# Kernel tuning notes

Measured on AMD Instinct MI355X. Metric: run time of the kernel, lower is better.

The kernel has to match this reference:

```python
import jax, jax.numpy as jnp
import numpy as np

NEG = 1e12  # matches torch code's -1e12 masking constant


def _rope_sincos(seq_len, dim, dtype):
    # SinusoidalPositionEmbedding with merge_mode='zero':
    # emb[n, i] pairs -> reshape to [n, dim] as [sin0, cos0, sin1, cos1, ...]
    pos = jnp.arange(seq_len, dtype=jnp.float32)
    inv = jnp.power(10000.0, -2.0 * jnp.arange(dim // 2, dtype=jnp.float32) / dim)
    ang = pos[:, None] * inv[None, :]            # [n, d/2]
    sin, cos = jnp.sin(ang), jnp.cos(ang)
    # cos_pos = pos[..., 1::2].repeat_interleave(2) == repeat(cos, 2)
    cos_pos = jnp.repeat(cos, 2, axis=-1).astype(dtype)  # [n, d]
    sin_pos = jnp.repeat(sin, 2, axis=-1).astype(dtype)  # [n, d]
    return sin_pos, cos_pos


def _rotate_half(x):
    # stack([-x[..., 1::2], x[..., ::2]], -1).reshape(x.shape)
    x2 = jnp.stack([-x[..., 1::2], x[..., ::2]], axis=-1)
    return x2.reshape(x.shape)


def setup_inputs() -> dict:
    key = jax.random.key(0)
    k1, k2, k3 = jax.random.split(key, 3)
    B, N, H = 8, 1024, 768
    heads, head_size = 12, 64
    inputs = jax.random.normal(k1, (B, N, H), dtype=jnp.float32)
    mask = jnp.ones((B, N), dtype=jnp.float32)
    W = jax.random.normal(k2, (H, heads * head_size * 2), dtype=jnp.float32) * (H ** -0.5)
    b = jnp.zeros((heads * head_size * 2,), dtype=jnp.float32)
    return {"inputs": inputs, "mask": mask, "W": W, "b": b}


def reference(inputs, mask, W, b):
    heads, head_size = 12, 64
    B, N, _ = inputs.shape
    x = inputs @ W + b                              # [B, N, heads*head_size*2]
    x = x.reshape(B, N, heads, 2 * head_size)       # split+stack over heads
    qw, kw = x[..., :head_size], x[..., head_size:]  # [B, N, heads, d]

    sin_pos, cos_pos = _rope_sincos(N, head_size, inputs.dtype)
    sin_pos = sin_pos[None, :, None, :]             # [1, N, 1, d]
    cos_pos = cos_pos[None, :, None, :]
    qw = qw * cos_pos + _rotate_half(qw) * sin_pos
    kw = kw * cos_pos + _rotate_half(kw) * sin_pos

    logits = jnp.einsum('bmhd,bnhd->bhmn', qw, kw)  # [B, heads, N, N]

    m1 = mask[:, None, :, None]                     # mask rows (axis ndim-2)
    m2 = mask[:, None, None, :]                     # mask cols (axis ndim-1)
    logits = logits * m1 + (-NEG) * (1.0 - m1)
    logits = logits * m2 + (-NEG) * (1.0 - m2)
    tril = jnp.tril(jnp.ones((N, N), dtype=logits.dtype), k=-1)
    logits = logits - tril * NEG                    # forbid end < start
    return logits / (head_size ** 0.5)
```

## Files before the change

kernel.cpp:

```cpp
#include <hip/hip_runtime.h>
#include <stdint.h>

#define NEGC 1000000000000.0f

using f32x4  = __attribute__((ext_vector_type(4))) float;
using short8 = __attribute__((ext_vector_type(8))) short;

typedef __attribute__((address_space(3))) uint32_t* lds_ptr_t;
typedef const __attribute__((address_space(1))) uint32_t* gptr_t;

__device__ __forceinline__ void gload_lds16(const void* g, const void* l) {
  __builtin_amdgcn_global_load_lds((gptr_t)g, (lds_ptr_t)l, 16, 0, 0);
}

__device__ __forceinline__ unsigned short f2bf(float f) {
  union { float f; uint32_t u; } v; v.f = f;
  uint32_t u = v.u;
  return (unsigned short)((u + 0x7fffu + ((u >> 16) & 1u)) >> 16);
}

__global__ __launch_bounds__(256) void k_prep(
    const float* __restrict__ in, unsigned short* __restrict__ inb,
    const float* __restrict__ W, unsigned short* __restrict__ Wt,
    float* __restrict__ ssin, float* __restrict__ scos) {
  __shared__ float tile[64][65];
  const int bx = blockIdx.x, t = threadIdx.x;
  if (bx < 6144) {
    int idx = bx * 256 + t;
    float4 v = ((const float4*)in)[idx];
    ushort4 o;
    o.x = f2bf(v.x); o.y = f2bf(v.y); o.z = f2bf(v.z); o.w = f2bf(v.w);
    ((ushort4*)inb)[idx] = o;
  } else if (bx < 6432) {
    int b = bx - 6144;
    int kb = b % 12, nb = b / 12;
    int c = t & 63, r0 = t >> 6;
#pragma unroll
    for (int p = 0; p < 16; ++p) {
      int r = r0 + p * 4;
      tile[r][c] = W[(size_t)(kb * 64 + r) * 1536 + nb * 64 + c];
    }
    __syncthreads();
#pragma unroll
    for (int p = 0; p < 16; ++p) {
      int n = r0 + p * 4;
      Wt[(size_t)(nb * 64 + n) * 768 + kb * 64 + c] = f2bf(tile[c][n]);
    }
  } else {
    int idx = (bx - 6432) * 256 + t;
    int m = idx >> 5, i = idx & 31;
    float inv = expf(-(float)i * (9.210340371976184f / 32.0f));
    float ang = (float)m * inv;
    ssin[idx] = sinf(ang);
    scos[idx] = cosf(ang);
  }
}

__global__ __launch_bounds__(256) void k_gemm1(
    const unsigned short* __restrict__ A,
    const unsigned short* __restrict__ Bt,
    const float* __restrict__ bias,
    const float* __restrict__ ssin, const float* __restrict__ scos,
    unsigned short* __restrict__ qb, unsigned short* __restrict__ kb) {
  __shared__ __align__(16) unsigned short As[128 * 64];
  __shared__ __align__(16) unsigned short Bs[128 * 64];
  const int tid = threadIdx.x;
  const int wave = tid >> 6, lane = tid & 63;
  const int wm = wave >> 1, wn = wave & 1;
  const int orig = blockIdx.x;
  const int xcd = orig & 7, idx = orig >> 3;
  const int mt8 = idx / 12;
  const int h   = idx - mt8 * 12;
  const int m0  = (xcd * 8 + mt8) * 128;
  const int j0  = h * 128;
  const int lr = lane >> 3, kc = lane & 7;

  f32x4 acc[4][4] = {};

  for (int kt = 0; kt < 12; ++kt) {
    const int k0 = kt * 64;
#pragma unroll
    for (int i = 0; i < 4; ++i) {
      int row = i * 32 + wave * 8 + lr;
      int gk = k0 + ((kc ^ (row & 7)) << 3);
      gload_lds16(&A[(size_t)(m0 + row) * 768 + gk], &As[(i * 32 + wave * 8) * 64]);
    }
#pragma unroll
    for (int i = 0; i < 4; ++i) {
      int row = i * 32 + wave * 8 + lr;
      int gk = k0 + ((kc ^ (row & 7)) << 3);
      gload_lds16(&Bt[(size_t)(j0 + row) * 768 + gk], &Bs[(i * 32 + wave * 8) * 64]);
    }
    asm volatile("s_waitcnt vmcnt(0)" ::: "memory");
    __syncthreads();
#pragma unroll
    for (int kh = 0; kh < 2; ++kh) {
      short8 af[4], bfr[4];
#pragma unroll
      for (int mt = 0; mt < 4; ++mt) {
        int row = wm * 64 + mt * 16 + (lane & 15);
        int cs = (kh * 4 + (lane >> 4)) ^ (row & 7);
        af[mt] = *(const short8*)&As[row * 64 + cs * 8];
      }
#pragma unroll
      for (int nt = 0; nt < 4; ++nt) {
        int row = wn * 64 + nt * 16 + (lane & 15);
        int cs = (kh * 4 + (lane >> 4)) ^ (row & 7);
        bfr[nt] = *(const short8*)&Bs[row * 64 + cs * 8];
      }
#pragma unroll
      for (int mt = 0; mt < 4; ++mt)
#pragma unroll
        for (int nt = 0; nt < 4; ++nt)
          acc[mt][nt] = __builtin_amdgcn_mfma_f32_16x16x32_bf16(af[mt], bfr[nt], acc[mt][nt], 0, 0, 0);
    }
    __syncthreads();
  }

  const int col = lane & 15, rquad = lane >> 4;
  unsigned short* dst = (wn == 0) ? qb : kb;
#pragma unroll
  for (int nt = 0; nt < 4; ++nt) {
    const int d = nt * 16 + col;
    const float bv = bias[j0 + wn * 64 + d];
    const int ifr = d >> 1;
    const float sgn = (d & 1) ? 1.0f : -1.0f;
#pragma unroll
    for (int mt = 0; mt < 4; ++mt) {
#pragma unroll
      for (int j = 0; j < 4; ++j) {
        int mg = m0 + wm * 64 + mt * 16 + rquad * 4 + j;
        int ms = mg & 1023, bi = mg >> 10;
        float v = acc[mt][nt][j] + bv;
        float p = __shfl_xor(v, 1, 64);
        float s = ssin[ms * 32 + ifr], cv = scos[ms * 32 + ifr];
        float r = v * cv + sgn * p * s;
        dst[(size_t)((bi * 12 + h) * 1024 + ms) * 64 + d] = f2bf(r);
      }
    }
  }
}

__global__ __launch_bounds__(256) void k_gemm2(
    const unsigned short* __restrict__ qb, const unsigned short* __restrict__ kbuf,
    const float* __restrict__ mask, float* __restrict__ out) {
  __shared__ __align__(16) unsigned short Qs[128 * 64];
  __shared__ __align__(16) unsigned short Ks[128 * 64];
  const int tid = threadIdx.x;
  const int wave = tid >> 6, lane = tid & 63;
  const int wm = wave >> 1, wn = wave & 1;
  const int orig = blockIdx.x;
  const int xcd = orig & 7, idx = orig >> 3;
  const int bh = xcd * 12 + (idx >> 6);
  const int tt = idx & 63;
  const int tm = tt >> 3, tn = tt & 7;
  const int b = bh / 12;
  const int lr = lane >> 3, kc = lane & 7;

  const unsigned short* qbase = qb   + (size_t)bh * (1024 * 64);
  const unsigned short* kbase = kbuf + (size_t)bh * (1024 * 64);

#pragma unroll
  for (int i = 0; i < 4; ++i) {
    int row = i * 32 + wave * 8 + lr;
    int gk = (kc ^ (row & 7)) << 3;
    gload_lds16(&qbase[(size_t)(tm * 128 + row) * 64 + gk], &Qs[(i * 32 + wave * 8) * 64]);
  }
#pragma unroll
  for (int i = 0; i < 4; ++i) {
    int row = i * 32 + wave * 8 + lr;
    int gk = (kc ^ (row & 7)) << 3;
    gload_lds16(&kbase[(size_t)(tn * 128 + row) * 64 + gk], &Ks[(i * 32 + wave * 8) * 64]);
  }
  asm volatile("s_waitcnt vmcnt(0)" ::: "memory");
  __syncthreads();

  f32x4 acc[4][4] = {};
#pragma unroll
  for (int kh = 0; kh < 2; ++kh) {
    short8 af[4], bfr[4];
#pragma unroll
    for (int mt = 0; mt < 4; ++mt) {
      int row = wm * 64 + mt * 16 + (lane & 15);
      int cs = (kh * 4 + (lane >> 4)) ^ (row & 7);
      af[mt] = *(const short8*)&Qs[row * 64 + cs * 8];
    }
#pragma unroll
    for (int nt = 0; nt < 4; ++nt) {
      int row = wn * 64 + nt * 16 + (lane & 15);
      int cs = (kh * 4 + (lane >> 4)) ^ (row & 7);
      bfr[nt] = *(const short8*)&Ks[row * 64 + cs * 8];
    }
#pragma unroll
    for (int mt = 0; mt < 4; ++mt)
#pragma unroll
      for (int nt = 0; nt < 4; ++nt)
        acc[mt][nt] = __builtin_amdgcn_mfma_f32_16x16x32_bf16(af[mt], bfr[nt], acc[mt][nt], 0, 0, 0);
  }

  float* obase = out + (size_t)bh * (1024 * 1024);
  const int col = lane & 15, rquad = lane >> 4;
  float m2v[4]; int ngv[4];
#pragma unroll
  for (int nt = 0; nt < 4; ++nt) {
    ngv[nt] = tn * 128 + wn * 64 + nt * 16 + col;
    m2v[nt] = mask[b * 1024 + ngv[nt]];
  }
#pragma unroll
  for (int mt = 0; mt < 4; ++mt) {
#pragma unroll
    for (int j = 0; j < 4; ++j) {
      int mg = tm * 128 + wm * 64 + mt * 16 + rquad * 4 + j;
      float m1 = mask[b * 1024 + mg];
      float* orow = obase + (size_t)mg * 1024;
#pragma unroll
      for (int nt = 0; nt < 4; ++nt) {
        float v = acc[mt][nt][j];
        v = v * m1 - NEGC * (1.0f - m1);
        v = v * m2v[nt] - NEGC * (1.0f - m2v[nt]);
        if (ngv[nt] < mg) v -= NEGC;
        orow[ngv[nt]] = v * 0.125f;
      }
    }
  }
}

extern "C" void kernel_launch(void* const* d_in, const int* in_sizes, int n_in,
                              void* d_out, int out_size, void* d_ws, size_t ws_size,
                              hipStream_t stream) {
  const float* inputs = (const float*)d_in[0];
  const float* mask   = (const float*)d_in[1];
  const float* W      = (const float*)d_in[2];
  const float* bias   = (const float*)d_in[3];
  float* out = (float*)d_out;
  char* ws = (char*)d_ws;

  float* ssin = (float*)(ws);
  float* scos = (float*)(ws + 131072);
  unsigned short* inA = (unsigned short*)(ws + 262144);
  unsigned short* Wt  = (unsigned short*)(ws + 262144 + 12582912);
  unsigned short* qb  = (unsigned short*)(ws + 262144 + 12582912 + 2359296);
  unsigned short* kb  = (unsigned short*)(ws + 262144 + 12582912 + 2359296 + 12582912);

  hipLaunchKernelGGL(k_prep, dim3(6560), dim3(256), 0, stream,
                     inputs, inA, W, Wt, ssin, scos);
  hipLaunchKernelGGL(k_gemm1, dim3(768), dim3(256), 0, stream,
                     inA, Wt, bias, ssin, scos, qb, kb);
  hipLaunchKernelGGL(k_gemm2, dim3(6144), dim3(256), 0, stream, qb, kb, mask, out);
}
```

Baseline: 130.8 us.

## Double-buffer LDS tiles in projection GEMM and use nontemporal logits stores

The projection GEMM now keeps two LDS buffers and issues the global-to-LDS loads for the next k-tile before computing on the current one, so load latency overlaps the MFMA work and one barrier per iteration is dropped. The logits kernel writes its output with nontemporal stores so the large fp32 output stream does not pollute the caches. In exchange, LDS use doubles to 64 KB per block, which may lower occupancy. The dominant cost is the roughly 400 MB output write, which these changes barely affect.

```diff
diff --git a/kernel.cpp b/kernel.cpp
--- a/kernel.cpp
+++ b/kernel.cpp
@@ -62,8 +62,8 @@
     const float* __restrict__ bias,
     const float* __restrict__ ssin, const float* __restrict__ scos,
     unsigned short* __restrict__ qb, unsigned short* __restrict__ kb) {
-  __shared__ __align__(16) unsigned short As[128 * 64];
-  __shared__ __align__(16) unsigned short Bs[128 * 64];
+  __shared__ __align__(16) unsigned short As[2][128 * 64];
+  __shared__ __align__(16) unsigned short Bs[2][128 * 64];
   const int tid = threadIdx.x;
   const int wave = tid >> 6, lane = tid & 63;
   const int wm = wave >> 1, wn = wave & 1;
@@ -77,22 +77,30 @@
 
   f32x4 acc[4][4] = {};
 
+#define STAGE1(buf, kt)                                                              \
+  {                                                                                  \
+    const int k0_ = (kt) * 64;                                                       \
+    _Pragma("unroll")                                                                \
+    for (int i = 0; i < 4; ++i) {                                                    \
+      int row = i * 32 + wave * 8 + lr;                                              \
+      int gk = k0_ + ((kc ^ (row & 7)) << 3);                                        \
+      gload_lds16(&A[(size_t)(m0 + row) * 768 + gk], &As[buf][(i * 32 + wave * 8) * 64]); \
+    }                                                                                \
+    _Pragma("unroll")                                                                \
+    for (int i = 0; i < 4; ++i) {                                                    \
+      int row = i * 32 + wave * 8 + lr;                                              \
+      int gk = k0_ + ((kc ^ (row & 7)) << 3);                                        \
+      gload_lds16(&Bt[(size_t)(j0 + row) * 768 + gk], &Bs[buf][(i * 32 + wave * 8) * 64]); \
+    }                                                                                \
+  }
+
+  STAGE1(0, 0);
+  asm volatile("s_waitcnt vmcnt(0)" ::: "memory");
+  __syncthreads();
+
+  int cur = 0;
   for (int kt = 0; kt < 12; ++kt) {
-    const int k0 = kt * 64;
-#pragma unroll
-    for (int i = 0; i < 4; ++i) {
-      int row = i * 32 + wave * 8 + lr;
-      int gk = k0 + ((kc ^ (row & 7)) << 3);
-      gload_lds16(&A[(size_t)(m0 + row) * 768 + gk], &As[(i * 32 + wave * 8) * 64]);
-    }
-#pragma unroll
-    for (int i = 0; i < 4; ++i) {
-      int row = i * 32 + wave * 8 + lr;
-      int gk = k0 + ((kc ^ (row & 7)) << 3);
-      gload_lds16(&Bt[(size_t)(j0 + row) * 768 + gk], &Bs[(i * 32 + wave * 8) * 64]);
-    }
-    asm volatile("s_waitcnt vmcnt(0)" ::: "memory");
-    __syncthreads();
+    if (kt < 11) STAGE1(cur ^ 1, kt + 1);
 #pragma unroll
     for (int kh = 0; kh < 2; ++kh) {
       short8 af[4], bfr[4];
@@ -100,13 +108,13 @@
       for (int mt = 0; mt < 4; ++mt) {
         int row = wm * 64 + mt * 16 + (lane & 15);
         int cs = (kh * 4 + (lane >> 4)) ^ (row & 7);
-        af[mt] = *(const short8*)&As[row * 64 + cs * 8];
+        af[mt] = *(const short8*)&As[cur][row * 64 + cs * 8];
       }
 #pragma unroll
       for (int nt = 0; nt < 4; ++nt) {
         int row = wn * 64 + nt * 16 + (lane & 15);
         int cs = (kh * 4 + (lane >> 4)) ^ (row & 7);
-        bfr[nt] = *(const short8*)&Bs[row * 64 + cs * 8];
+        bfr[nt] = *(const short8*)&Bs[cur][row * 64 + cs * 8];
       }
 #pragma unroll
       for (int mt = 0; mt < 4; ++mt)
@@ -114,8 +122,13 @@
         for (int nt = 0; nt < 4; ++nt)
           acc[mt][nt] = __builtin_amdgcn_mfma_f32_16x16x32_bf16(af[mt], bfr[nt], acc[mt][nt], 0, 0, 0);
     }
-    __syncthreads();
-  }
+    if (kt < 11) {
+      asm volatile("s_waitcnt vmcnt(0)" ::: "memory");
+      __syncthreads();
+      cur ^= 1;
+    }
+  }
+#undef STAGE1
 
   const int col = lane & 15, rquad = lane >> 4;
   unsigned short* dst = (wn == 0) ? qb : kb;
@@ -219,7 +232,7 @@
         v = v * m1 - NEGC * (1.0f - m1);
         v = v * m2v[nt] - NEGC * (1.0f - m2v[nt]);
         if (ngv[nt] < mg) v -= NEGC;
-        orow[ngv[nt]] = v * 0.125f;
+        __builtin_nontemporal_store(v * 0.125f, &orow[ngv[nt]]);
       }
     }
   }
```

Result: slower. 164.5 us (+25.8%).

## Make logits kernel loop over key tiles with double-buffered K prefetch

Applied to the files above, without the earlier changes.

Each block of the logits kernel now keeps one Q tile in LDS and loops over all eight key tiles, prefetching the next K tile into a second LDS buffer while computing and writing the current one. The grid shrinks from one block per output tile to one block per query tile row. The aim is to reuse Q loads and hide K load latency behind MFMA work and output stores. The risk is fewer resident blocks in flight to saturate the write-bound output traffic.

```diff
diff --git a/kernel.cpp b/kernel.cpp
--- a/kernel.cpp
+++ b/kernel.cpp
@@ -145,20 +145,31 @@
     const unsigned short* __restrict__ qb, const unsigned short* __restrict__ kbuf,
     const float* __restrict__ mask, float* __restrict__ out) {
   __shared__ __align__(16) unsigned short Qs[128 * 64];
-  __shared__ __align__(16) unsigned short Ks[128 * 64];
+  __shared__ __align__(16) unsigned short Ks[2][128 * 64];
   const int tid = threadIdx.x;
   const int wave = tid >> 6, lane = tid & 63;
   const int wm = wave >> 1, wn = wave & 1;
   const int orig = blockIdx.x;
   const int xcd = orig & 7, idx = orig >> 3;
-  const int bh = xcd * 12 + (idx >> 6);
-  const int tt = idx & 63;
-  const int tm = tt >> 3, tn = tt & 7;
+  const int bh = xcd * 12 + (idx >> 3);
+  const int tm = idx & 7;
   const int b = bh / 12;
   const int lr = lane >> 3, kc = lane & 7;
 
   const unsigned short* qbase = qb   + (size_t)bh * (1024 * 64);
   const unsigned short* kbase = kbuf + (size_t)bh * (1024 * 64);
+  float* obase = out + (size_t)bh * (1024 * 1024);
+
+#define STAGEK(buf, tn_)                                                             \
+  {                                                                                  \
+    _Pragma("unroll")                                                                \
+    for (int i = 0; i < 4; ++i) {                                                    \
+      int row = i * 32 + wave * 8 + lr;                                              \
+      int gk = (kc ^ (row & 7)) << 3;                                                \
+      gload_lds16(&kbase[(size_t)((tn_) * 128 + row) * 64 + gk],                     \
+                  &Ks[buf][(i * 32 + wave * 8) * 64]);                               \
+    }                                                                                \
+  }
 
 #pragma unroll
   for (int i = 0; i < 4; ++i) {
@@ -166,63 +177,69 @@
     int gk = (kc ^ (row & 7)) << 3;
     gload_lds16(&qbase[(size_t)(tm * 128 + row) * 64 + gk], &Qs[(i * 32 + wave * 8) * 64]);
   }
-#pragma unroll
-  for (int i = 0; i < 4; ++i) {
-    int row = i * 32 + wave * 8 + lr;
-    int gk = (kc ^ (row & 7)) << 3;
-    gload_lds16(&kbase[(size_t)(tn * 128 + row) * 64 + gk], &Ks[(i * 32 + wave * 8) * 64]);
-  }
+  STAGEK(0, 0);
   asm volatile("s_waitcnt vmcnt(0)" ::: "memory");
   __syncthreads();
 
-  f32x4 acc[4][4] = {};
-#pragma unroll
-  for (int kh = 0; kh < 2; ++kh) {
-    short8 af[4], bfr[4];
+  const int col = lane & 15, rquad = lane >> 4;
+  int cur = 0;
+  for (int tn = 0; tn < 8; ++tn) {
+    if (tn < 7) STAGEK(cur ^ 1, tn + 1);
+
+    f32x4 acc[4][4] = {};
+#pragma unroll
+    for (int kh = 0; kh < 2; ++kh) {
+      short8 af[4], bfr[4];
+#pragma unroll
+      for (int mt = 0; mt < 4; ++mt) {
+        int row = wm * 64 + mt * 16 + (lane & 15);
+        int cs = (kh * 4 + (lane >> 4)) ^ (row & 7);
+        af[mt] = *(const short8*)&Qs[row * 64 + cs * 8];
+      }
+#pragma unroll
+      for (int nt = 0; nt < 4; ++nt) {
+        int row = wn * 64 + nt * 16 + (lane & 15);
+        int cs = (kh * 4 + (lane >> 4)) ^ (row & 7);
+        bfr[nt] = *(const short8*)&Ks[cur][row * 64 + cs * 8];
+      }
+#pragma unroll
+      for (int mt = 0; mt < 4; ++mt)
+#pragma unroll
+        for (int nt = 0; nt < 4; ++nt)
+          acc[mt][nt] = __builtin_amdgcn_mfma_f32_16x16x32_bf16(af[mt], bfr[nt], acc[mt][nt], 0, 0, 0);
+    }
+
+    if (tn < 7) {
+      asm volatile("s_waitcnt vmcnt(0)" ::: "memory");
+      __syncthreads();
+    }
+
+    float m2v[4]; int ngv[4];
+#pragma unroll
+    for (int nt = 0; nt < 4; ++nt) {
+      ngv[nt] = tn * 128 + wn * 64 + nt * 16 + col;
+      m2v[nt] = mask[b * 1024 + ngv[nt]];
+    }
 #pragma unroll
     for (int mt = 0; mt < 4; ++mt) {
-      int row = wm * 64 + mt * 16 + (lane & 15);
-      int cs = (kh * 4 + (lane >> 4)) ^ (row & 7);
-      af[mt] = *(const short8*)&Qs[row * 64 + cs * 8];
-    }
-#pragma unroll
-    for (int nt = 0; nt < 4; ++nt) {
-      int row = wn * 64 + nt * 16 + (lane & 15);
-      int cs = (kh * 4 + (lane >> 4)) ^ (row & 7);
-      bfr[nt] = *(const short8*)&Ks[row * 64 + cs * 8];
-    }
-#pragma unroll
-    for (int mt = 0; mt < 4; ++mt)
-#pragma unroll
-      for (int nt = 0; nt < 4; ++nt)
-        acc[mt][nt] = __builtin_amdgcn_mfma_f32_16x16x32_bf16(af[mt], bfr[nt], acc[mt][nt], 0, 0, 0);
-  }
-
-  float* obase = out + (size_t)bh * (1024 * 1024);
-  const int col = lane & 15, rquad = lane >> 4;
-  float m2v[4]; int ngv[4];
-#pragma unroll
-  for (int nt = 0; nt < 4; ++nt) {
-    ngv[nt] = tn * 128 + wn * 64 + nt * 16 + col;
-    m2v[nt] = mask[b * 1024 + ngv[nt]];
-  }
-#pragma unroll
-  for (int mt = 0; mt < 4; ++mt) {
-#pragma unroll
-    for (int j = 0; j < 4; ++j) {
-      int mg = tm * 128 + wm * 64 + mt * 16 + rquad * 4 + j;
-      float m1 = mask[b * 1024 + mg];
-      float* orow = obase + (size_t)mg * 1024;
-#pragma unroll
-      for (int nt = 0; nt < 4; ++nt) {
-        float v = acc[mt][nt][j];
-        v = v * m1 - NEGC * (1.0f - m1);
-        v = v * m2v[nt] - NEGC * (1.0f - m2v[nt]);
-        if (ngv[nt] < mg) v -= NEGC;
-        orow[ngv[nt]] = v * 0.125f;
-      }
-    }
-  }
+#pragma unroll
+      for (int j = 0; j < 4; ++j) {
+        int mg = tm * 128 + wm * 64 + mt * 16 + rquad * 4 + j;
+        float m1 = mask[b * 1024 + mg];
+        float* orow = obase + (size_t)mg * 1024;
+#pragma unroll
+        for (int nt = 0; nt < 4; ++nt) {
+          float v = acc[mt][nt][j];
+          v = v * m1 - NEGC * (1.0f - m1);
+          v = v * m2v[nt] - NEGC * (1.0f - m2v[nt]);
+          if (ngv[nt] < mg) v -= NEGC;
+          orow[ngv[nt]] = v * 0.125f;
+        }
+      }
+    }
+    cur ^= 1;
+  }
+#undef STAGEK
 }
 
 extern "C" void kernel_launch(void* const* d_in, const int* in_sizes, int n_in,
@@ -246,5 +263,5 @@
                      inputs, inA, W, Wt, ssin, scos);
   hipLaunchKernelGGL(k_gemm1, dim3(768), dim3(256), 0, stream,
                      inA, Wt, bias, ssin, scos, qb, kb);
-  hipLaunchKernelGGL(k_gemm2, dim3(6144), dim3(256), 0, stream, qb, kb, mask, out);
-}
+  hipLaunchKernelGGL(k_gemm2, dim3(768), dim3(256), 0, stream, qb, kb, mask, out);
+}
```

New measurement: 138.4 us. +5.8%, slower.
